# Optimization experiments

Measured on AMD Instinct MI355X. Metric: run time of the kernel, lower is better.

## Reference

```python
import jax, jax.numpy as jnp
import numpy as np

N = 50000      # nodes
E = 800000     # edges (before self-loops)
IN = 256       # in_channels
HID = 16       # hidden_channels per head
HEADS = 8
OUT = 64       # out_channels (classes)
NEG_SLOPE = 0.2  # PyG GATConv leaky_relu slope


def setup_inputs() -> dict:
    key = jax.random.key(0)
    ks = jax.random.split(key, 10)
    x = jax.random.normal(ks[0], (N, IN), jnp.float32)
    edge_index = jax.random.randint(ks[1], (2, E), 0, N, dtype=jnp.int32)
    g = lambda k, shape: jax.random.normal(k, shape, jnp.float32) * (1.0 / np.sqrt(shape[0]))
    W1 = g(ks[2], (IN, HEADS * HID))
    a_src1 = jax.random.normal(ks[3], (HEADS, HID), jnp.float32) * 0.1
    a_dst1 = jax.random.normal(ks[4], (HEADS, HID), jnp.float32) * 0.1
    b1 = jnp.zeros((HEADS * HID,), jnp.float32)
    W2 = g(ks[5], (HEADS * HID, OUT))
    a_src2 = jax.random.normal(ks[6], (1, OUT), jnp.float32) * 0.1
    a_dst2 = jax.random.normal(ks[7], (1, OUT), jnp.float32) * 0.1
    b2 = jnp.zeros((OUT,), jnp.float32)
    return {"x": x, "edge_index": edge_index, "W1": W1, "a_src1": a_src1,
            "a_dst1": a_dst1, "b1": b1, "W2": W2, "a_src2": a_src2,
            "a_dst2": a_dst2, "b2": b2}


def gat_conv(x, src, dst, W, a_s, a_d, b, heads, concat):
    # x: [n, f]; edges src->dst; attention softmax over incoming edges of dst
    n = x.shape[0]
    h = (x @ W).reshape(n, heads, -1)                 # [n, H, d]
    al_s = jnp.einsum('nhd,hd->nh', h, a_s)           # [n, H]
    al_d = jnp.einsum('nhd,hd->nh', h, a_d)
    e = jax.nn.leaky_relu(al_s[src] + al_d[dst], negative_slope=NEG_SLOPE)  # [E, H]
    m = jax.ops.segment_max(e, dst, num_segments=n)   # stable scatter-softmax
    ex = jnp.exp(e - m[dst])
    den = jax.ops.segment_sum(ex, dst, num_segments=n)
    alpha = ex / (den[dst] + 1e-16)                   # [E, H]
    out = jax.ops.segment_sum(h[src] * alpha[:, :, None], dst, num_segments=n)  # [n, H, d]
    out = out.reshape(n, -1) if concat else out.mean(axis=1)
    return out + b


def reference(x, edge_index, W1, a_src1, a_dst1, b1, W2, a_src2, a_dst2, b2):
    # inference mode: dropout disabled. PyG GATConv adds self-loops by default.
    n = x.shape[0]
    loop = jnp.arange(n, dtype=edge_index.dtype)
    ei = jnp.concatenate([edge_index, jnp.stack([loop, loop])], axis=1)
    src, dst = ei[0], ei[1]
    h = gat_conv(x, src, dst, W1, a_src1, a_dst1, b1, HEADS, True)
    h = jax.nn.elu(h)
    h = gat_conv(h, src, dst, W2, a_src2, a_dst2, b2, 1, False)
    return jax.nn.log_softmax(h, axis=1)
```

## Files before the change

### kernel.cpp

```cpp
#include <hip/hip_runtime.h>
#include <hip/hip_bf16.h>


typedef __attribute__((ext_vector_type(8))) short short8;
typedef __attribute__((ext_vector_type(4))) float f4;
typedef __attribute__((ext_vector_type(2))) float float2v;

#define NCHUNK 64
#define NRANGE 4
#define RSIZE 16384
#define CONVB 80

__device__ __forceinline__ unsigned short f2bf(float f) {
  unsigned int u = __builtin_bit_cast(unsigned int, f);
  u += 0x7fffu + ((u >> 16) & 1u);
  return (unsigned short)(u >> 16);
}
__device__ __forceinline__ float bf2f(unsigned short h) {
  unsigned int u = ((unsigned int)h) << 16;
  return __builtin_bit_cast(float, u);
}

__device__ __forceinline__ unsigned char f2fp8(float f) {
  unsigned int u = __builtin_bit_cast(unsigned int, f);
  unsigned int s = (u >> 24) & 0x80u;
  float a = fabsf(f);
  a = fminf(a, 448.f);
  if (a < 0.015625f) {
    int m = (int)rintf(a * 512.f);
    return (unsigned char)(s | (unsigned)m);
  }
  unsigned int ub = __builtin_bit_cast(unsigned int, a);
  ub += 0xFFFFFu + ((ub >> 20) & 1u);
  unsigned int e = (ub >> 23) - 120u;
  unsigned int m = (ub >> 20) & 7u;
  if (e > 15u) { e = 15u; m = 6u; }
  return (unsigned char)(s | (e << 3) | m);
}

__global__ __launch_bounds__(512) void hist_kernel(const int* __restrict__ ei,
                                                   int* __restrict__ hist,
                                                   const float* __restrict__ W1,
                                                   const float* __restrict__ W2,
                                                   unsigned short* __restrict__ Wt1,
                                                   unsigned short* __restrict__ Wt2,
                                                   int E, int N, int ET, int CS) {
  if (blockIdx.x >= NCHUNK * NRANGE) {
    int i = (blockIdx.x - NCHUNK * NRANGE) * 512 + threadIdx.x;
    if (i < 128 * 256) {
      int n = i >> 8, k = i & 255;
      Wt1[i] = f2bf(W1[k * 128 + n]);
    } else {
      int j = i - 128 * 256;
      if (j < 64 * 128) {
        int n = j >> 7, k = j & 127;
        Wt2[j] = f2bf(W2[k * 64 + n]);
      }
    }
    return;
  }
  __shared__ int lh[RSIZE];
  const int c = blockIdx.x & (NCHUNK - 1);
  const int r = blockIdx.x >> 6;
  const int base = r * RSIZE;
  for (int i = threadIdx.x; i < RSIZE; i += 512) lh[i] = 0;
  __syncthreads();
  const int e0 = c * CS, e1 = min(e0 + CS, ET);
  for (int e = e0 + threadIdx.x; e < e1; e += 512) {
    int d = (e < E) ? ei[E + e] : (e - E);
    unsigned dl = (unsigned)(d - base);
    if (dl < RSIZE) atomicAdd(&lh[dl], 1);
  }
  __syncthreads();
  for (int i = threadIdx.x; i < RSIZE; i += 512) {
    int d = base + i;
    if (d < N) hist[c * N + d] = lh[i];
  }
}

__global__ __launch_bounds__(256) void colscan_kernel(int* __restrict__ hist,
                                                      int* __restrict__ deg, int N) {
  int d = blockIdx.x * 256 + threadIdx.x;
  if (d >= N) return;
  int run = 0;
#pragma unroll 8
  for (int c = 0; c < NCHUNK; ++c) {
    int v = hist[c * N + d];
    hist[c * N + d] = run;
    run += v;
  }
  deg[d] = run;
}

__global__ __launch_bounds__(1024) void scan1_kernel(const int* __restrict__ deg,
                                                     int* __restrict__ rowptr,
                                                     int* __restrict__ bsum, int N) {
  __shared__ int wtot[16];
  const int lane = threadIdx.x & 63, wid = threadIdx.x >> 6;
  int i = blockIdx.x * 1024 + threadIdx.x;
  int v = (i < N) ? deg[i] : 0;
  int incl = v;
#pragma unroll
  for (int off = 1; off < 64; off <<= 1) {
    int t = __shfl_up(incl, off, 64);
    if (lane >= off) incl += t;
  }
  if (lane == 63) wtot[wid] = incl;
  __syncthreads();
  int woff = 0;
#pragma unroll
  for (int w = 0; w < 16; ++w) woff += (w < wid) ? wtot[w] : 0;
  if (i < N) rowptr[i] = woff + incl - v;
  if (threadIdx.x == 1023) bsum[blockIdx.x] = woff + incl;
}

__global__ __launch_bounds__(256) void scan3_kernel(int* __restrict__ rowptr,
                                                    const int* __restrict__ bsum,
                                                    int N, int ET) {
  int lane = threadIdx.x & 63;
  int g = blockIdx.x >> 2;
  int bv = (lane < g) ? bsum[lane] : 0;
#pragma unroll
  for (int off = 32; off; off >>= 1) bv += __shfl_xor(bv, off, 64);
  int i = blockIdx.x * 256 + threadIdx.x;
  if (i < N) rowptr[i] += bv;
  if (i == N) rowptr[N] = ET;
}

__global__ __launch_bounds__(512) void scatter2_kernel(const int* __restrict__ ei,
                                                       const int* __restrict__ hist,
                                                       const int* __restrict__ rowptr,
                                                       int* __restrict__ csr_src,
                                                       int E, int N, int ET, int CS) {
  __shared__ int lh[RSIZE];
  const int c = blockIdx.x & (NCHUNK - 1);
  const int r = blockIdx.x >> 6;
  const int base = r * RSIZE;
  for (int i = threadIdx.x; i < RSIZE; i += 512) {
    int d = base + i;
    lh[i] = (d < N) ? (rowptr[d] + hist[c * N + d]) : 0;
  }
  __syncthreads();
  const int e0 = c * CS, e1 = min(e0 + CS, ET);
  for (int e = e0 + threadIdx.x; e < e1; e += 512) {
    int s, d;
    if (e < E) { s = ei[e]; d = ei[E + e]; }
    else       { s = e - E; d = s; }
    unsigned dl = (unsigned)(d - base);
    if (dl < RSIZE) {
      int slot = atomicAdd(&lh[dl], 1);
      csr_src[slot] = s;
    }
  }
}

__global__ __launch_bounds__(256) void gemm1_mfma(const float* __restrict__ X,
                                                  const unsigned short* __restrict__ Wt,
                                                  const float* __restrict__ as1,
                                                  const float* __restrict__ ad1,
                                                  unsigned char* __restrict__ H,
                                                  float* __restrict__ als,
                                                  float* __restrict__ ald,
                                                  int M) {
  const int t = threadIdx.x;
  const int wv = t >> 6, ln = t & 63;
  const int ml = ln & 15, q = ln >> 4;
  const int ch = blockIdx.x & 1;
  const int r0 = (blockIdx.x >> 1) * 64 + wv * 16;
  const int arow = min(r0 + ml, M - 1);
  const float* xp = X + (size_t)arow * 256 + q * 8;

  short8 av[8];
#pragma unroll
  for (int s = 0; s < 8; ++s) {
    float4 a0 = *(const float4*)(xp + s * 32);
    float4 a1 = *(const float4*)(xp + s * 32 + 4);
    av[s][0] = (short)f2bf(a0.x); av[s][1] = (short)f2bf(a0.y);
    av[s][2] = (short)f2bf(a0.z); av[s][3] = (short)f2bf(a0.w);
    av[s][4] = (short)f2bf(a1.x); av[s][5] = (short)f2bf(a1.y);
    av[s][6] = (short)f2bf(a1.z); av[s][7] = (short)f2bf(a1.w);
  }

  const unsigned short* wb = Wt + (size_t)(ch * 64 + ml) * 256 + q * 8;

  f4 acc[4];
#pragma unroll
  for (int b = 0; b < 4; ++b) acc[b] = (f4)0.f;

#pragma unroll
  for (int s = 0; s < 8; ++s) {
#pragma unroll
    for (int b = 0; b < 4; ++b) {
      short8 bfr = *(const short8*)(wb + (size_t)(b * 16) * 256 + s * 32);
      acc[b] = __builtin_amdgcn_mfma_f32_16x16x32_bf16(av[s], bfr, acc[b], 0, 0, 0);
    }
  }

#pragma unroll
  for (int i = 0; i < 4; ++i) {
    int rr = r0 + q * 4 + i;
    bool ok = rr < M;
    if (ok) {
#pragma unroll
      for (int b = 0; b < 4; ++b)
        H[(size_t)rr * 128 + ch * 64 + b * 16 + ml] = f2fp8(acc[b][i]);
    }
#pragma unroll
    for (int b = 0; b < 4; ++b) {
      float ps = acc[b][i] * as1[ch * 64 + b * 16 + ml];
      float pd = acc[b][i] * ad1[ch * 64 + b * 16 + ml];
#pragma unroll
      for (int off = 1; off < 16; off <<= 1) {
        ps += __shfl_xor(ps, off, 16);
        pd += __shfl_xor(pd, off, 16);
      }
      if (ok && ml == b) {
        als[(size_t)rr * 8 + ch * 4 + b] = ps;
        ald[(size_t)rr * 8 + ch * 4 + b] = pd;
      }
    }
  }
}

__global__ __launch_bounds__(256) void gemm2_mfma(const unsigned short* __restrict__ Xb,
                                                  const unsigned short* __restrict__ Wt,
                                                  const float* __restrict__ as2,
                                                  const float* __restrict__ ad2,
                                                  unsigned char* __restrict__ H,
                                                  float* __restrict__ als,
                                                  float* __restrict__ ald,
                                                  int M) {
  const int t = threadIdx.x;
  const int wv = t >> 6, ln = t & 63;
  const int ml = ln & 15, q = ln >> 4;
  const int r0 = blockIdx.x * 64 + wv * 16;
  const int arow = min(r0 + ml, M - 1);
  const unsigned short* xp = Xb + (size_t)arow * 128 + q * 8;

  short8 av[4];
#pragma unroll
  for (int s = 0; s < 4; ++s) av[s] = *(const short8*)(xp + s * 32);

  const unsigned short* wb = Wt + (size_t)ml * 128 + q * 8;

  f4 acc[4];
#pragma unroll
  for (int b = 0; b < 4; ++b) acc[b] = (f4)0.f;

#pragma unroll
  for (int s = 0; s < 4; ++s) {
#pragma unroll
    for (int b = 0; b < 4; ++b) {
      short8 bfr = *(const short8*)(wb + (size_t)(b * 16) * 128 + s * 32);
      acc[b] = __builtin_amdgcn_mfma_f32_16x16x32_bf16(av[s], bfr, acc[b], 0, 0, 0);
    }
  }

#pragma unroll
  for (int i = 0; i < 4; ++i) {
    int rr = r0 + q * 4 + i;
    bool ok = rr < M;
    if (ok) {
#pragma unroll
      for (int b = 0; b < 4; ++b)
        H[(size_t)rr * 64 + b * 16 + ml] = f2fp8(acc[b][i]);
    }
    float ps = 0.f, pd = 0.f;
#pragma unroll
    for (int b = 0; b < 4; ++b) {
      ps += acc[b][i] * as2[b * 16 + ml];
      pd += acc[b][i] * ad2[b * 16 + ml];
    }
#pragma unroll
    for (int off = 1; off < 16; off <<= 1) {
      ps += __shfl_xor(ps, off, 16);
      pd += __shfl_xor(pd, off, 16);
    }
    if (ok && ml == 0) { als[rr] = ps; ald[rr] = pd; }
  }
}

__global__ __launch_bounds__(256) void attn1_kernel(
    const unsigned char* __restrict__ h1, const float* __restrict__ als,
    const float* __restrict__ ald, const float* __restrict__ b1,
    const int* __restrict__ rowptr, const int* __restrict__ csr_src,
    unsigned short* __restrict__ helu, int N) {
  int d = __builtin_amdgcn_readfirstlane(
      (blockIdx.x * blockDim.x + threadIdx.x) >> 6);
  int lane = threadIdx.x & 63;
  if (d >= N) return;
  const int hh = lane >> 3;
  const int hw = lane & 7;
  const int ew = lane >> 3;
  const float aldp = ald[d * 8 + hw];
  const int beg = rowptr[d], end = rowptr[d + 1];
  const unsigned char* h1l = h1 + 2 * lane;
  float den = 0.f, ax = 0.f, ay = 0.f;

  for (int p0 = beg; p0 < end; p0 += 8) {
    int idx = p0 + ew;
    int se = csr_src[idx < end ? idx : end - 1];
    float v = als[se * 8 + hw] + aldp;
    v = fmaxf(v, 0.2f * v);
    float w = (idx < end) ? __expf(v) : 0.f;
#pragma unroll
    for (int j = 0; j < 4; ++j) {
      float wj = __shfl(w, j * 8 + hh);
      int sj = __shfl(se, j * 8);
      unsigned short pk = *(const unsigned short*)(h1l + (size_t)sj * 128);
      float2v g = __builtin_amdgcn_cvt_pk_f32_fp8(pk, false);
      den += wj; ax += wj * g.x; ay += wj * g.y;
    }
    if (p0 + 4 < end) {
#pragma unroll
      for (int j = 4; j < 8; ++j) {
        float wj = __shfl(w, j * 8 + hh);
        int sj = __shfl(se, j * 8);
        unsigned short pk = *(const unsigned short*)(h1l + (size_t)sj * 128);
        float2v g = __builtin_amdgcn_cvt_pk_f32_fp8(pk, false);
        den += wj; ax += wj * g.x; ay += wj * g.y;
      }
    }
  }

  float inv = 1.0f / (den + 1e-16f);
  float2 bb = *(const float2*)(b1 + 2 * lane);
  float o0 = ax * inv + bb.x;
  float o1 = ay * inv + bb.y;
  o0 = o0 > 0.f ? o0 : __expf(o0) - 1.0f;
  o1 = o1 > 0.f ? o1 : __expf(o1) - 1.0f;
  ushort2 ov; ov.x = f2bf(o0); ov.y = f2bf(o1);
  *(ushort2*)(helu + (size_t)d * 128 + 2 * lane) = ov;
}

__global__ __launch_bounds__(256) void attn2_kernel(
    const unsigned char* __restrict__ h2, const float* __restrict__ als,
    const float* __restrict__ ald, const float* __restrict__ b2,
    const int* __restrict__ rowptr, const int* __restrict__ csr_src,
    float* __restrict__ out, int N) {
  int d = __builtin_amdgcn_readfirstlane(
      (blockIdx.x * blockDim.x + threadIdx.x) >> 6);
  int lane = threadIdx.x & 63;
  if (d >= N) return;
  const float aldd = ald[d];
  const int beg = rowptr[d], end = rowptr[d + 1];
  const unsigned char* h2l = h2 + lane;
  float den = 0.f, acc = 0.f;

  for (int p0 = beg; p0 < end; p0 += 64) {
    int idx = p0 + lane;
    int se = csr_src[idx < end ? idx : end - 1];
    float v = als[se] + aldd;
    v = fmaxf(v, 0.2f * v);
    float w = (idx < end) ? __expf(v) : 0.f;
    int cnt = min(64, end - p0);
    for (int j0 = 0; j0 < cnt; j0 += 4) {
#pragma unroll
      for (int j = 0; j < 4; ++j) {
        float wj = __shfl(w, j0 + j);
        int sj = __shfl(se, j0 + j);
        float g = __builtin_amdgcn_cvt_f32_fp8(h2l[(size_t)sj * 64], 0);
        den += wj; acc += wj * g;
      }
    }
  }

  float z = acc / (den + 1e-16f) + b2[lane];
  float zm = z;
#pragma unroll
  for (int off = 32; off; off >>= 1) zm = fmaxf(zm, __shfl_xor(zm, off, 64));
  float ex = __expf(z - zm), se2 = ex;
#pragma unroll
  for (int off = 32; off; off >>= 1) se2 += __shfl_xor(se2, off, 64);
  out[(size_t)d * 64 + lane] = z - zm - __logf(se2);
}

extern "C" void kernel_launch(void* const* d_in, const int* in_sizes, int n_in,
                              void* d_out, int out_size, void* d_ws, size_t ws_size,
                              hipStream_t stream) {
  const int N = in_sizes[0] / 256;
  const int E = in_sizes[1] / 2;
  const int ET = E + N;
  const int CS = (ET + NCHUNK - 1) / NCHUNK;
  const int NB = (N + 1023) / 1024;

  const float* x   = (const float*)d_in[0];
  const int*   ei  = (const int*)d_in[1];
  const float* W1  = (const float*)d_in[2];
  const float* as1 = (const float*)d_in[3];
  const float* ad1 = (const float*)d_in[4];
  const float* b1  = (const float*)d_in[5];
  const float* W2  = (const float*)d_in[6];
  const float* as2 = (const float*)d_in[7];
  const float* ad2 = (const float*)d_in[8];
  const float* b2  = (const float*)d_in[9];
  float* out = (float*)d_out;

  char* p = (char*)d_ws;
  unsigned char* h1f8 = (unsigned char*)p; p += (size_t)N * 128;
  unsigned char* h2f8 = h1f8;
  unsigned short* helu = (unsigned short*)p; p += (size_t)NCHUNK * N * 4;
  int* hist = (int*)helu;
  unsigned short* Wt1  = (unsigned short*)p; p += (size_t)128 * 256 * 2;
  unsigned short* Wt2  = (unsigned short*)p; p += (size_t)64 * 128 * 2;
  float* als1 = (float*)p; p += (size_t)N * 8 * 4;
  float* ald1 = (float*)p; p += (size_t)N * 8 * 4;
  float* als2 = (float*)p; p += (size_t)N * 4;
  float* ald2 = (float*)p; p += (size_t)N * 4;
  int* deg     = (int*)p; p += (size_t)N * 4;
  int* rowptr  = (int*)p; p += (size_t)(N + 1) * 4;
  int* bsum    = (int*)p; p += 64 * 4;
  int* csr_src = (int*)p; p += (size_t)ET * 4;

  hist_kernel<<<NCHUNK * NRANGE + CONVB, 512, 0, stream>>>(ei, hist, W1, W2, Wt1, Wt2,
                                                           E, N, ET, CS);
  colscan_kernel<<<(N + 255) / 256, 256, 0, stream>>>(hist, deg, N);
  scan1_kernel<<<NB, 1024, 0, stream>>>(deg, rowptr, bsum, N);
  scan3_kernel<<<(N + 256) / 256, 256, 0, stream>>>(rowptr, bsum, N, ET);
  scatter2_kernel<<<NCHUNK * NRANGE, 512, 0, stream>>>(ei, hist, rowptr, csr_src, E, N, ET, CS);

  gemm1_mfma<<<2 * ((N + 63) / 64), 256, 0, stream>>>(x, Wt1, as1, ad1, h1f8, als1, ald1, N);
  attn1_kernel<<<(N + 3) / 4, 256, 0, stream>>>(h1f8, als1, ald1, b1, rowptr, csr_src, helu, N);

  gemm2_mfma<<<(N + 63) / 64, 256, 0, stream>>>(helu, Wt2, as2, ad2, h2f8, als2, ald2, N);
  attn2_kernel<<<(N + 3) / 4, 256, 0, stream>>>(h2f8, als2, ald2, b2, rowptr, csr_src, out, N);
}
```

Baseline: 273.9 us.

## Stage GEMM operands through padded LDS with double-buffered A tiles

```diff
diff --git a/kernel.cpp b/kernel.cpp
--- a/kernel.cpp
+++ b/kernel.cpp
@@ -10,6 +10,10 @@
 #define NRANGE 4
 #define RSIZE 16384
 #define CONVB 80
+
+#define A1PAD 72
+#define B1PAD 264
+#define G2PAD 136
 
 __device__ __forceinline__ unsigned short f2bf(float f) {
   unsigned int u = __builtin_bit_cast(unsigned int, f);
@@ -162,38 +166,79 @@
                                                   float* __restrict__ als,
                                                   float* __restrict__ ald,
                                                   int M) {
+  __shared__ unsigned short Bs[64 * B1PAD];
+  __shared__ unsigned short As[2][64 * A1PAD];
   const int t = threadIdx.x;
-  const int wv = t >> 6, ln = t & 63;
+  const int ln = t & 63;
+  const int wv = t >> 6;
   const int ml = ln & 15, q = ln >> 4;
   const int ch = blockIdx.x & 1;
-  const int r0 = (blockIdx.x >> 1) * 64 + wv * 16;
-  const int arow = min(r0 + ml, M - 1);
-  const float* xp = X + (size_t)arow * 256 + q * 8;
-
-  short8 av[8];
-#pragma unroll
-  for (int s = 0; s < 8; ++s) {
-    float4 a0 = *(const float4*)(xp + s * 32);
-    float4 a1 = *(const float4*)(xp + s * 32 + 4);
-    av[s][0] = (short)f2bf(a0.x); av[s][1] = (short)f2bf(a0.y);
-    av[s][2] = (short)f2bf(a0.z); av[s][3] = (short)f2bf(a0.w);
-    av[s][4] = (short)f2bf(a1.x); av[s][5] = (short)f2bf(a1.y);
-    av[s][6] = (short)f2bf(a1.z); av[s][7] = (short)f2bf(a1.w);
-  }
-
-  const unsigned short* wb = Wt + (size_t)(ch * 64 + ml) * 256 + q * 8;
+  const int rb = (blockIdx.x >> 1) * 64;
+  const int r0 = rb + wv * 16;
+  const int alr = wv * 16 + ml;
+
+  int srow[4], skg[4];
+#pragma unroll
+  for (int i = 0; i < 4; ++i) {
+    int g = i * 256 + t;
+    srow[i] = g >> 4;
+    skg[i] = g & 15;
+  }
+
+  float4 astg[4];
+#pragma unroll
+  for (int i = 0; i < 4; ++i)
+    astg[i] = *(const float4*)(X + (size_t)min(rb + srow[i], M - 1) * 256 + skg[i] * 4);
+
+#pragma unroll
+  for (int i = 0; i < 8; ++i) {
+    int g = i * 256 + t;
+    int brow = g >> 5, bc = g & 31;
+    *(short8*)&Bs[brow * B1PAD + bc * 8] =
+        *(const short8*)(Wt + (size_t)(ch * 64 + brow) * 256 + bc * 8);
+  }
+
+#pragma unroll
+  for (int i = 0; i < 4; ++i) {
+    ushort4 pk;
+    pk.x = f2bf(astg[i].x); pk.y = f2bf(astg[i].y);
+    pk.z = f2bf(astg[i].z); pk.w = f2bf(astg[i].w);
+    *(ushort4*)&As[0][srow[i] * A1PAD + skg[i] * 4] = pk;
+  }
+  __syncthreads();
 
   f4 acc[4];
 #pragma unroll
   for (int b = 0; b < 4; ++b) acc[b] = (f4)0.f;
 
 #pragma unroll
-  for (int s = 0; s < 8; ++s) {
-#pragma unroll
-    for (int b = 0; b < 4; ++b) {
-      short8 bfr = *(const short8*)(wb + (size_t)(b * 16) * 256 + s * 32);
-      acc[b] = __builtin_amdgcn_mfma_f32_16x16x32_bf16(av[s], bfr, acc[b], 0, 0, 0);
-    }
+  for (int s = 0; s < 4; ++s) {
+    const int buf = s & 1;
+    if (s < 3) {
+#pragma unroll
+      for (int i = 0; i < 4; ++i)
+        astg[i] = *(const float4*)(X + (size_t)min(rb + srow[i], M - 1) * 256 +
+                                   (s + 1) * 64 + skg[i] * 4);
+    }
+#pragma unroll
+    for (int kk = 0; kk < 2; ++kk) {
+      short8 av = *(const short8*)&As[buf][alr * A1PAD + kk * 32 + q * 8];
+#pragma unroll
+      for (int b = 0; b < 4; ++b) {
+        short8 bfr = *(const short8*)&Bs[(b * 16 + ml) * B1PAD + s * 64 + kk * 32 + q * 8];
+        acc[b] = __builtin_amdgcn_mfma_f32_16x16x32_bf16(av, bfr, acc[b], 0, 0, 0);
+      }
+    }
+    if (s < 3) {
+#pragma unroll
+      for (int i = 0; i < 4; ++i) {
+        ushort4 pk;
+        pk.x = f2bf(astg[i].x); pk.y = f2bf(astg[i].y);
+        pk.z = f2bf(astg[i].z); pk.w = f2bf(astg[i].w);
+        *(ushort4*)&As[buf ^ 1][srow[i] * A1PAD + skg[i] * 4] = pk;
+      }
+    }
+    __syncthreads();
   }
 
 #pragma unroll
@@ -230,18 +275,31 @@
                                                   float* __restrict__ als,
                                                   float* __restrict__ ald,
                                                   int M) {
+  __shared__ unsigned short Asl[64 * G2PAD];
+  __shared__ unsigned short Bsl[64 * G2PAD];
   const int t = threadIdx.x;
-  const int wv = t >> 6, ln = t & 63;
+  const int ln = t & 63;
+  const int wv = t >> 6;
   const int ml = ln & 15, q = ln >> 4;
-  const int r0 = blockIdx.x * 64 + wv * 16;
-  const int arow = min(r0 + ml, M - 1);
-  const unsigned short* xp = Xb + (size_t)arow * 128 + q * 8;
+  const int rb = blockIdx.x * 64;
+  const int r0 = rb + wv * 16;
+  const int alr = wv * 16 + ml;
+
+#pragma unroll
+  for (int i = 0; i < 4; ++i) {
+    int g = i * 256 + t;
+    int row = g >> 4, kg = g & 15;
+    *(short8*)&Asl[row * G2PAD + kg * 8] =
+        *(const short8*)(Xb + (size_t)min(rb + row, M - 1) * 128 + kg * 8);
+    *(short8*)&Bsl[row * G2PAD + kg * 8] =
+        *(const short8*)(Wt + (size_t)row * 128 + kg * 8);
+  }
+  __syncthreads();
 
   short8 av[4];
 #pragma unroll
-  for (int s = 0; s < 4; ++s) av[s] = *(const short8*)(xp + s * 32);
-
-  const unsigned short* wb = Wt + (size_t)ml * 128 + q * 8;
+  for (int s = 0; s < 4; ++s)
+    av[s] = *(const short8*)&Asl[alr * G2PAD + s * 32 + q * 8];
 
   f4 acc[4];
 #pragma unroll
@@ -251,7 +309,7 @@
   for (int s = 0; s < 4; ++s) {
 #pragma unroll
     for (int b = 0; b < 4; ++b) {
-      short8 bfr = *(const short8*)(wb + (size_t)(b * 16) * 128 + s * 32);
+      short8 bfr = *(const short8*)&Bsl[(b * 16 + ml) * G2PAD + s * 32 + q * 8];
       acc[b] = __builtin_amdgcn_mfma_f32_16x16x32_bf16(av[s], bfr, acc[b], 0, 0, 0);
     }
   }
```

Result: faster. 253.9 us (-7.3%).
